# Performance work log

Measured on AMD Instinct MI355X. Metric: run time of the kernel, lower is better.

Reference implementation:

```python
import jax, jax.numpy as jnp
import numpy as np

B, S, D, H, DK, F, L, V = 4, 128, 512, 8, 64, 2048, 2, 32000
N = B * S  # nodes per side (enc and dec each)


def _pe():
    pos = np.arange(S, dtype=np.float32)[:, None]
    div = np.exp(-np.log(10000.0) * np.arange(0, D, 2, dtype=np.float32) / D)
    pe = np.zeros((S, D), dtype=np.float32)
    pe[:, 0::2] = np.sin(pos * div)
    pe[:, 1::2] = np.cos(pos * div)
    return jnp.asarray(np.tile(pe, (B, 1)))  # [N, D]


def _ln(x, g, b, eps=1e-5):
    mu = jnp.mean(x, -1, keepdims=True)
    var = jnp.mean(jnp.square(x - mu), -1, keepdims=True)
    return g * (x - mu) * jax.lax.rsqrt(var + eps) + b


def _edge_attn(q, k, v, src, dst, n_dst):
    # src_dot_dst('k','q','score') then scaled_exp, then src_mul_edge + sum scatter
    s = jnp.sum(k[src] * q[dst], -1, keepdims=True) / np.float32(np.sqrt(DK))  # [E,H,1]
    s = jnp.exp(jnp.clip(s, -10.0, 10.0))
    wv = jax.ops.segment_sum(v[src] * s, dst, num_segments=n_dst)  # [n_dst,H,DK]
    z = jax.ops.segment_sum(s, dst, num_segments=n_dst)            # [n_dst,H,1]
    return wv / z


def _attn_block(x_q, x_kv, Wq, Wk, Wv, Wo, src, dst):
    q = (x_q @ Wq).reshape(-1, H, DK)
    k = (x_kv @ Wk).reshape(-1, H, DK)
    v = (x_kv @ Wv).reshape(-1, H, DK)
    o = _edge_attn(q, k, v, src, dst, x_q.shape[0]).reshape(-1, D)
    return o @ Wo


def _forward(p, src_tok, tgt_tok, ee_src, ee_dst, dd_src, dd_dst, ed_src, ed_dst):
    (src_emb, tgt_emb, enc_Wqkv, enc_Wo, enc_ln1, enc_W1, enc_b1, enc_W2, enc_b2,
     enc_ln2, enc_lnf, dec_Wqkv, dec_Wo, dec_ln1, dec_cWq, dec_cWkv, dec_cWo,
     dec_ln2, dec_W1, dec_b1, dec_W2, dec_b2, dec_ln3, dec_lnf, gen_W, gen_b) = p
    pe = _pe()
    scale = np.float32(np.sqrt(D))
    x_e = src_emb[src_tok].reshape(N, D) * scale + pe  # token + positional embed
    x_d = tgt_emb[tgt_tok].reshape(N, D) * scale + pe
    for l in range(L):  # encoder layers (ee edges)
        xn = _ln(x_e, enc_ln1[l, 0], enc_ln1[l, 1])
        x_e = x_e + _attn_block(xn, xn, enc_Wqkv[l, 0], enc_Wqkv[l, 1], enc_Wqkv[l, 2], enc_Wo[l], ee_src, ee_dst)
        xn = _ln(x_e, enc_ln2[l, 0], enc_ln2[l, 1])
        x_e = x_e + jax.nn.relu(xn @ enc_W1[l] + enc_b1[l]) @ enc_W2[l] + enc_b2[l]
    x_e = _ln(x_e, enc_lnf[0], enc_lnf[1])
    for l in range(L):  # decoder layers: self (dd) then cross (ed)
        xn = _ln(x_d, dec_ln1[l, 0], dec_ln1[l, 1])
        x_d = x_d + _attn_block(xn, xn, dec_Wqkv[l, 0], dec_Wqkv[l, 1], dec_Wqkv[l, 2], dec_Wo[l], dd_src, dd_dst)
        xn = _ln(x_d, dec_ln2[l, 0], dec_ln2[l, 1])
        x_d = x_d + _attn_block(xn, x_e, dec_cWq[l], dec_cWkv[l, 0], dec_cWkv[l, 1], dec_cWo[l], ed_src, ed_dst)
        xn = _ln(x_d, dec_ln3[l, 0], dec_ln3[l, 1])
        x_d = x_d + jax.nn.relu(xn @ dec_W1[l] + dec_b1[l]) @ dec_W2[l] + dec_b2[l]
    x_d = _ln(x_d, dec_lnf[0], dec_lnf[1])
    return jax.nn.log_softmax(x_d @ gen_W + gen_b, axis=-1)  # generator


def setup_inputs():
    key = jax.random.key(0)
    ks = iter(jax.random.split(key, 32))
    w = lambda *shape: jax.random.normal(next(ks), shape, jnp.float32) * 0.02
    lnp = lambda n: jnp.tile(jnp.stack([jnp.ones(D), jnp.zeros(D)])[None], (n, 1, 1))
    # structured edge lists: per-sentence blocks
    i, j = np.meshgrid(np.arange(S), np.arange(S), indexing='ij')  # src pos, dst pos
    base = (np.arange(B)[:, None] * S).astype(np.int32)
    full_s = (base + i.ravel()[None, :]).ravel().astype(np.int32)
    full_d = (base + j.ravel()[None, :]).ravel().astype(np.int32)
    m = i.ravel() <= j.ravel()  # causal mask for dec self-attention
    dd_s = (base + i.ravel()[m][None, :]).ravel().astype(np.int32)
    dd_d = (base + j.ravel()[m][None, :]).ravel().astype(np.int32)
    k1, k2 = jax.random.split(next(ks))
    return dict(
        src_emb=w(V, D), tgt_emb=w(V, D),
        enc_Wqkv=w(L, 3, D, D), enc_Wo=w(L, D, D), enc_ln1=lnp(L),
        enc_W1=w(L, D, F), enc_b1=jnp.zeros((L, F)), enc_W2=w(L, F, D),
        enc_b2=jnp.zeros((L, D)), enc_ln2=lnp(L), enc_lnf=lnp(1)[0],
        dec_Wqkv=w(L, 3, D, D), dec_Wo=w(L, D, D), dec_ln1=lnp(L),
        dec_cWq=w(L, D, D), dec_cWkv=w(L, 2, D, D), dec_cWo=w(L, D, D), dec_ln2=lnp(L),
        dec_W1=w(L, D, F), dec_b1=jnp.zeros((L, F)), dec_W2=w(L, F, D),
        dec_b2=jnp.zeros((L, D)), dec_ln3=lnp(L), dec_lnf=lnp(1)[0],
        gen_W=w(D, V), gen_b=jnp.zeros((V,)),
        src_tok=jax.random.randint(k1, (B, S), 0, V, jnp.int32),
        tgt_tok=jax.random.randint(k2, (B, S), 0, V, jnp.int32),
        ee_src=jnp.asarray(full_s), ee_dst=jnp.asarray(full_d),
        dd_src=jnp.asarray(dd_s), dd_dst=jnp.asarray(dd_d),
        ed_src=jnp.asarray(full_s), ed_dst=jnp.asarray(full_d),
    )


def reference(src_emb, tgt_emb, enc_Wqkv, enc_Wo, enc_ln1, enc_W1, enc_b1, enc_W2,
              enc_b2, enc_ln2, enc_lnf, dec_Wqkv, dec_Wo, dec_ln1, dec_cWq,
              dec_cWkv, dec_cWo, dec_ln2, dec_W1, dec_b1, dec_W2, dec_b2,
              dec_ln3, dec_lnf, gen_W, gen_b, src_tok, tgt_tok, ee_src, ee_dst,
              dd_src, dd_dst, ed_src, ed_dst):
    p = (src_emb, tgt_emb, enc_Wqkv, enc_Wo, enc_ln1, enc_W1, enc_b1, enc_W2,
         enc_b2, enc_ln2, enc_lnf, dec_Wqkv, dec_Wo, dec_ln1, dec_cWq, dec_cWkv,
         dec_cWo, dec_ln2, dec_W1, dec_b1, dec_W2, dec_b2, dec_ln3, dec_lnf,
         gen_W, gen_b)
    return _forward(p, src_tok, tgt_tok, ee_src, ee_dst, dd_src, dd_dst, ed_src, ed_dst)
```

## Files before the change

### kernel.cpp

```cpp
#include <hip/hip_runtime.h>
#include <cstddef>

constexpr int cB = 4, cS = 128, cD = 512, cH = 8, cDK = 64, cF = 2048, cL = 2, cV = 32000;
constexpr int cN = cB * cS;

typedef __attribute__((ext_vector_type(8)))  short short8;
typedef __attribute__((ext_vector_type(4)))  float f32x4;
typedef __attribute__((ext_vector_type(16))) float f32x16;

__device__ __forceinline__ short f2bf(float x) {
    unsigned u = __builtin_bit_cast(unsigned, x);
    unsigned r = (u + 0x7fffu + ((u >> 16) & 1u)) >> 16;
    return (short)r;
}
__device__ __forceinline__ short f2h(float x) {
    return __builtin_bit_cast(short, (_Float16)x);
}
__device__ __forceinline__ float h2f(short s) {
    return (float)__builtin_bit_cast(_Float16, s);
}

__device__ __forceinline__ void bar_lgkm() {
    asm volatile("s_waitcnt lgkmcnt(0)" ::: "memory");
    __builtin_amdgcn_s_barrier();
    asm volatile("" ::: "memory");
}

__global__ __launch_bounds__(256) void embed_k(const float* __restrict__ e0,
                                               const int* __restrict__ t0,
                                               float* __restrict__ X0,
                                               const float* __restrict__ e1,
                                               const int* __restrict__ t1,
                                               float* __restrict__ X1)
{
    const float* emb = blockIdx.z ? e1 : e0;
    const int* tok   = blockIdx.z ? t1 : t0;
    float* X         = blockIdx.z ? X1 : X0;
    int n = blockIdx.x;
    int tid = threadIdx.x;
    int t = tok[n];
    int pos = n & (cS - 1);
    const float scale = 22.62741699796952f;
    for (int d = tid; d < cD; d += 256) {
        int i2 = d & ~1;
        float div = expf(-9.210340371976184f * (float)i2 / (float)cD);
        float arg = (float)pos * div;
        float p = (d & 1) ? cosf(arg) : sinf(arg);
        X[(long)n * cD + d] = emb[(long)t * cD + d] * scale + p;
    }
}

__global__ __launch_bounds__(256) void ln_k(const float* __restrict__ X,
                                            const float* __restrict__ g,
                                            const float* __restrict__ bta,
                                            short* __restrict__ Yb)
{
    __shared__ float red[256];
    int row = blockIdx.x, tid = threadIdx.x;
    const float* x = X + (long)row * cD;
    float v0 = x[tid], v1 = x[tid + 256];

    red[tid] = v0 + v1;
    __syncthreads();
    for (int st = 128; st > 0; st >>= 1) { if (tid < st) red[tid] += red[tid + st]; __syncthreads(); }
    float mu = red[0] * (1.0f / (float)cD);
    __syncthreads();

    float d0 = v0 - mu, d1 = v1 - mu;
    red[tid] = d0 * d0 + d1 * d1;
    __syncthreads();
    for (int st = 128; st > 0; st >>= 1) { if (tid < st) red[tid] += red[tid + st]; __syncthreads(); }
    float var = red[0] * (1.0f / (float)cD);
    float rs = rsqrtf(var + 1e-5f);

    Yb[(long)row * cD + tid]       = f2bf(g[tid]       * d0 * rs + bta[tid]);
    Yb[(long)row * cD + tid + 256] = f2bf(g[tid + 256] * d1 * rs + bta[tid + 256]);
}

struct TCP { const float* s[24]; };

__global__ __launch_bounds__(256) void tconv_k(TCP ptrs, short* __restrict__ dst,
                                               int K, int N)
{
    __shared__ float t[64][65];
    const float* s = ptrs.s[blockIdx.z];
    short* d = dst + (long)blockIdx.z * K * N;
    int k0 = blockIdx.y * 64, n0 = blockIdx.x * 64;
    int tid = threadIdx.x;
    const f32x4* s4 = (const f32x4*)s;
#pragma unroll
    for (int i = 0; i < 4; i++) {
        int lin = tid + i * 256;
        int r = lin >> 4, c4 = lin & 15;
        f32x4 v = s4[(long)(k0 + r) * (N >> 2) + (n0 >> 2) + c4];
        t[r][c4 * 4 + 0] = v[0]; t[r][c4 * 4 + 1] = v[1];
        t[r][c4 * 4 + 2] = v[2]; t[r][c4 * 4 + 3] = v[3];
    }
    __syncthreads();
#pragma unroll
    for (int i = 0; i < 2; i++) {
        int lin = tid + i * 256;
        int r = lin >> 3, c8 = lin & 7;
        short8 o;
#pragma unroll
        for (int j = 0; j < 8; j++) o[j] = f2bf(t[c8 * 8 + j][r]);
        *(short8*)&d[(long)(n0 + r) * K + k0 + c8 * 8] = o;
    }
}

template <int MR, int NR, bool LNF>
__global__ __launch_bounds__(512) void gemm8_k(
    const short* __restrict__ Abf, const float* __restrict__ Af,
    const float* __restrict__ lng, const float* __restrict__ lnb,
    const float* __restrict__ Af2, const float* __restrict__ lng2,
    const float* __restrict__ lnb2, int zsplit,
    const short* __restrict__ Bt,
    const float* __restrict__ bias, const float* __restrict__ res,
    float* __restrict__ C, short* __restrict__ Cb,
    int N, int K, int relu, long aStride, long btStride, long cStride)
{
    constexpr int BM = MR * 32, BN = NR * 32, PITCH = 136;
    constexpr int ACH = (BM * 128) / (8 * 512);
    constexpr int BCH = (BN * 128) / (8 * 512);
    static_assert(ACH >= 1 && BCH >= 1, "tile too small");
    __shared__ short As[2][BM * PITCH];
    __shared__ short Bs[2][BN * PITCH];
    __shared__ float red[4][64][MR * NR * 4];
    __shared__ float mu_s[BM], rs_s[BM];
    __shared__ float gb_s[2][LNF ? 512 : 8];

    const int z = blockIdx.z;
    const float* Afz = (LNF && z >= zsplit) ? Af2 : Af;
    const float* gz  = (LNF && z >= zsplit) ? lng2 : lng;
    const float* bz  = (LNF && z >= zsplit) ? lnb2 : lnb;
    const short* Am = Abf ? (Abf + (long)z * aStride) : nullptr;
    const short* Bm = Bt + (long)z * btStride;
    int tid = threadIdx.x;
    int lane = tid & 63, wid = tid >> 6;
    int grp = wid >> 2, quad = wid & 3;
    int wr = quad >> 1, wc = quad & 1;
    int m0 = blockIdx.y * BM, n0 = blockIdx.x * BN;
    int lrow = lane & 15, koff = (lane >> 4) * 8;
    const int Kh = K >> 1;

    if constexpr (LNF) {
        constexpr int TPR = 512 / BM;
        int r = tid / TPR, sub = tid % TPR;
        const f32x4* row4 = (const f32x4*)(Afz + (long)(m0 + r) * K);
        float s = 0.f, s2 = 0.f;
        for (int i = sub; i < (K >> 2); i += TPR) {
            f32x4 v = row4[i];
            s  += v[0] + v[1] + v[2] + v[3];
            s2 += v[0] * v[0] + v[1] * v[1] + v[2] * v[2] + v[3] * v[3];
        }
#pragma unroll
        for (int o = TPR >> 1; o > 0; o >>= 1) {
            s += __shfl_xor(s, o); s2 += __shfl_xor(s2, o);
        }
        if (sub == 0) {
            float mu = s / (float)K;
            float var = s2 / (float)K - mu * mu;
            mu_s[r] = mu; rs_s[r] = rsqrtf(var + 1e-5f);
        }
        if (tid < 512) { gb_s[0][tid] = gz[tid]; gb_s[1][tid] = bz[tid]; }
        bar_lgkm();
    }

    f32x4 acc[MR][NR];
#pragma unroll
    for (int m = 0; m < MR; m++)
#pragma unroll
        for (int n = 0; n < NR; n++) acc[m][n] = f32x4{0.f, 0.f, 0.f, 0.f};

    short8 qa0[ACH], qa1[ACH], qb0[BCH], qb1[BCH];

    auto stage = [&](int step, short8 (&qa)[ACH], short8 (&qb)[BCH]) {
#pragma unroll
        for (int i = 0; i < ACH; i++) {
            int lin = tid + i * 512, r = lin >> 4, c8 = lin & 15;
            int kg = (c8 < 8) ? (step * 64 + c8 * 8) : (Kh + step * 64 + (c8 - 8) * 8);
            if constexpr (LNF) {
                const f32x4* p = (const f32x4*)(Afz + (long)(m0 + r) * K + kg);
                f32x4 f0 = p[0], f1 = p[1];
                float mu = mu_s[r], rs = rs_s[r];
                short8 o;
#pragma unroll
                for (int j = 0; j < 4; j++)
                    o[j] = f2bf((f0[j] - mu) * rs * gb_s[0][kg + j] + gb_s[1][kg + j]);
#pragma unroll
                for (int j = 0; j < 4; j++)
                    o[4 + j] = f2bf((f1[j] - mu) * rs * gb_s[0][kg + 4 + j] + gb_s[1][kg + 4 + j]);
                qa[i] = o;
            } else {
                qa[i] = *(const short8*)&Am[(long)(m0 + r) * K + kg];
            }
        }
#pragma unroll
        for (int i = 0; i < BCH; i++) {
            int lin = tid + i * 512, r = lin >> 4, c8 = lin & 15;
            int kg = (c8 < 8) ? (step * 64 + c8 * 8) : (Kh + step * 64 + (c8 - 8) * 8);
            qb[i] = *(const short8*)&Bm[(long)(n0 + r) * K + kg];
        }
    };
    auto writeT = [&](int buf, short8 (&qa)[ACH], short8 (&qb)[BCH]) {
#pragma unroll
        for (int i = 0; i < ACH; i++) {
            int lin = tid + i * 512, r = lin >> 4, c8 = lin & 15;
            *(short8*)&As[buf][r * PITCH + c8 * 8] = qa[i];
        }
#pragma unroll
        for (int i = 0; i < BCH; i++) {
            int lin = tid + i * 512, r = lin >> 4, c8 = lin & 15;
            *(short8*)&Bs[buf][r * PITCH + c8 * 8] = qb[i];
        }
    };
    auto mfmaStep = [&](int buf) {
#pragma unroll
        for (int kk2 = 0; kk2 < 2; kk2++) {
            int kk = grp * 64 + kk2 * 32;
            short8 a[MR], b[NR];
#pragma unroll
            for (int m = 0; m < MR; m++)
                a[m] = *(const short8*)&As[buf][(wr * MR * 16 + m * 16 + lrow) * PITCH + kk + koff];
#pragma unroll
            for (int n = 0; n < NR; n++)
                b[n] = *(const short8*)&Bs[buf][(wc * NR * 16 + n * 16 + lrow) * PITCH + kk + koff];
#pragma unroll
            for (int m = 0; m < MR; m++)
#pragma unroll
                for (int n = 0; n < NR; n++)
                    acc[m][n] = __builtin_amdgcn_mfma_f32_16x16x32_bf16(a[m], b[n], acc[m][n], 0, 0, 0);
        }
    };

    const int steps = K >> 7;
    stage(0, qa0, qb0);
    if (steps > 1) stage(1, qa1, qb1);

    int st = 0;
    for (;;) {
        writeT(0, qa0, qb0);
        if (st + 2 < steps) stage(st + 2, qa0, qb0);
        bar_lgkm();
        mfmaStep(0);
        st++; if (st >= steps) break;

        writeT(1, qa1, qb1);
        if (st + 2 < steps) stage(st + 2, qa1, qb1);
        bar_lgkm();
        mfmaStep(1);
        st++; if (st >= steps) break;
    }

    __syncthreads();
    if (grp == 1) {
#pragma unroll
        for (int m = 0; m < MR; m++)
#pragma unroll
            for (int n = 0; n < NR; n++)
#pragma unroll
                for (int j = 0; j < 4; j++)
                    red[quad][lane][(m * NR + n) * 4 + j] = acc[m][n][j];
    }
    __syncthreads();
    if (grp == 0) {
#pragma unroll
        for (int m = 0; m < MR; m++) {
            int rbase = m0 + wr * MR * 16 + m * 16 + (lane >> 4) * 4;
#pragma unroll
            for (int n = 0; n < NR; n++) {
                int col = n0 + wc * NR * 16 + n * 16 + (lane & 15);
                float bv = bias ? bias[col] : 0.f;
#pragma unroll
                for (int j = 0; j < 4; j++) {
                    long row = rbase + j;
                    long off = row * N + col + (long)z * cStride;
                    float v = acc[m][n][j] + red[quad][lane][(m * NR + n) * 4 + j] + bv;
                    if (res)  v += res[off];
                    if (relu) v = fmaxf(v, 0.f);
                    if (C)  C[off] = v;
                    if (Cb) Cb[off] = f2bf(v);
                }
            }
        }
    }
}

__global__ __launch_bounds__(256) void attn_k(const short* __restrict__ Qb,
                                              const short* __restrict__ Kb,
                                              const short* __restrict__ Vb,
                                              short* __restrict__ Ob,
                                              int causMask, long sQKV, long sO)
{
    __shared__ short q_s[64 * 72];
    __shared__ short k_s[128 * 72];
    __shared__ short vt_s[64 * 128];
    __shared__ short p_s[64 * 136];
    __shared__ float z_s[64];

    int tid = threadIdx.x, lane = tid & 63, wid = tid >> 6;
    int lr = lane & 15, lg = lane >> 4;
    int h = blockIdx.x, b = blockIdx.y;
    int stream = blockIdx.z >> 1, dstBase = (blockIdx.z & 1) * 64;
    int causal = (causMask >> stream) & 1;
    const short* Q = Qb + (long)stream * sQKV;
    const short* Km = Kb + (long)stream * sQKV;
    const short* Vm = Vb + (long)stream * sQKV;
    short* O = Ob + (long)stream * sO;
    const int RS = cH * cDK;
    long qbase = ((long)b * cS + dstBase) * RS + h * cDK;
    long kbase = ((long)b * cS) * RS + h * cDK;

#pragma unroll
    for (int i = 0; i < 2; i++) {
        int lin = tid + i * 256, t = lin >> 3, c8 = lin & 7;
        *(short8*)&q_s[t * 72 + c8 * 8] = *(const short8*)&Q[qbase + (long)t * RS + c8 * 8];
    }
#pragma unroll
    for (int i = 0; i < 4; i++) {
        int lin = tid + i * 256, t = lin >> 3, c8 = lin & 7;
        *(short8*)&k_s[t * 72 + c8 * 8] = *(const short8*)&Km[kbase + (long)t * RS + c8 * 8];
    }
#pragma unroll
    for (int i = 0; i < 4; i++) {
        int lin = tid + i * 256, src = lin >> 3, c8 = lin & 7;
        short8 v = *(const short8*)&Vm[kbase + (long)src * RS + c8 * 8];
#pragma unroll
        for (int j = 0; j < 8; j++) {
            int dk = c8 * 8 + j;
            int g = (src >> 3) ^ (dk >> 3);
            vt_s[dk * 128 + g * 8 + (src & 7)] = v[j];
        }
    }
    bar_lgkm();

    f32x4 sacc[8];
#pragma unroll
    for (int n = 0; n < 8; n++) sacc[n] = f32x4{0.f, 0.f, 0.f, 0.f};
#pragma unroll
    for (int kk = 0; kk < 64; kk += 32) {
        short8 a = *(const short8*)&q_s[(wid * 16 + lr) * 72 + kk + lg * 8];
#pragma unroll
        for (int n = 0; n < 8; n++) {
            short8 bf = *(const short8*)&k_s[(n * 16 + lr) * 72 + kk + lg * 8];
            sacc[n] = __builtin_amdgcn_mfma_f32_16x16x32_bf16(a, bf, sacc[n], 0, 0, 0);
        }
    }
    float z[4] = {0.f, 0.f, 0.f, 0.f};
#pragma unroll
    for (int n = 0; n < 8; n++) {
        int src = n * 16 + lr;
#pragma unroll
        for (int j = 0; j < 4; j++) {
            int dst = dstBase + wid * 16 + lg * 4 + j;
            float s = sacc[n][j] * 0.125f;
            s = __expf(fminf(fmaxf(s, -10.f), 10.f));
            if (causal && src > dst) s = 0.f;
            sacc[n][j] = s;
            z[j] += s;
        }
    }
#pragma unroll
    for (int j = 0; j < 4; j++) {
        z[j] += __shfl_xor(z[j], 1); z[j] += __shfl_xor(z[j], 2);
        z[j] += __shfl_xor(z[j], 4); z[j] += __shfl_xor(z[j], 8);
    }
#pragma unroll
    for (int n = 0; n < 8; n++) {
        int src = n * 16 + lr;
#pragma unroll
        for (int j = 0; j < 4; j++)
            p_s[(wid * 16 + lg * 4 + j) * 136 + src] = f2bf(sacc[n][j]);
    }
    if (lr == 0) {
#pragma unroll
        for (int j = 0; j < 4; j++) z_s[wid * 16 + lg * 4 + j] = z[j];
    }
    bar_lgkm();

    f32x4 oacc[4];
#pragma unroll
    for (int n = 0; n < 4; n++) oacc[n] = f32x4{0.f, 0.f, 0.f, 0.f};
#pragma unroll
    for (int kk = 0; kk < 128; kk += 32) {
        int dkr = wid * 16 + lr;
        int g = ((kk >> 3) + lg) ^ (dkr >> 3);
        short8 a = *(const short8*)&vt_s[dkr * 128 + g * 8];
#pragma unroll
        for (int n = 0; n < 4; n++) {
            short8 bf = *(const short8*)&p_s[(n * 16 + lr) * 136 + kk + lg * 8];
            oacc[n] = __builtin_amdgcn_mfma_f32_16x16x32_bf16(a, bf, oacc[n], 0, 0, 0);
        }
    }
#pragma unroll
    for (int n = 0; n < 4; n++) {
        int dl = n * 16 + lr;
        float zz = z_s[dl];
#pragma unroll
        for (int j = 0; j < 4; j++) {
            int dk = wid * 16 + lg * 4 + j;
            O[qbase + (long)dl * RS + dk] = f2bf(oacc[n][j] / zz);
        }
    }
}

__global__ __launch_bounds__(256) void gen32_k(
    const short* __restrict__ A, const float* __restrict__ Bw,
    const float* __restrict__ bias, short* __restrict__ Ch, int N, int K)
{
    constexpr int PA = 72, PB = 132;
    __shared__ short As[128 * PA];
    __shared__ float Bsf[64 * PB];

    int bx = blockIdx.x, by = blockIdx.y;
    {
        int nb = gridDim.x * gridDim.y;
        int bid = by * gridDim.x + bx;
        int w = (bid & 7) * (nb >> 3) + (bid >> 3);
        by = w % gridDim.y; bx = w / gridDim.y;
    }
    int tid = threadIdx.x;
    int lane = tid & 63, wid = tid >> 6;
    int wr = wid >> 1, wc = wid & 1;
    int m0 = by * 128, n0 = bx * 128;
    int l31 = lane & 31, l5 = lane >> 5;

    f32x16 acc[2][2];
#pragma unroll
    for (int m = 0; m < 2; m++)
#pragma unroll
        for (int n = 0; n < 2; n++)
#pragma unroll
            for (int r = 0; r < 16; r++) acc[m][n][r] = 0.f;

    short8 qa0[4], qa1[4];
    f32x4  qb0[8], qb1[8];
    auto stage = [&](int k0, short8 (&qa)[4], f32x4 (&qb)[8]) {
#pragma unroll
        for (int i = 0; i < 4; i++) {
            int lin = tid + i * 256, r = lin >> 3, c8 = lin & 7;
            qa[i] = *(const short8*)&A[(long)(m0 + r) * K + k0 + c8 * 8];
        }
#pragma unroll
        for (int i = 0; i < 8; i++) {
            int lin = tid + i * 256, kr = lin >> 5, c4 = lin & 31;
            qb[i] = *(const f32x4*)&Bw[(long)(k0 + kr) * N + n0 + c4 * 4];
        }
    };
    auto writeT = [&](short8 (&qa)[4], f32x4 (&qb)[8]) {
#pragma unroll
        for (int i = 0; i < 4; i++) {
            int lin = tid + i * 256, r = lin >> 3, c8 = lin & 7;
            *(short8*)&As[r * PA + c8 * 8] = qa[i];
        }
#pragma unroll
        for (int i = 0; i < 8; i++) {
            int lin = tid + i * 256, kr = lin >> 5, c4 = lin & 31;
            *(f32x4*)&Bsf[kr * PB + c4 * 4] = qb[i];
        }
    };
    auto mfmaStep = [&]() {
#pragma unroll
        for (int kk = 0; kk < 64; kk += 16) {
            short8 a[2], b[2];
#pragma unroll
            for (int m = 0; m < 2; m++)
                a[m] = *(const short8*)&As[(wr * 64 + m * 32 + l31) * PA + kk + l5 * 8];
#pragma unroll
            for (int n = 0; n < 2; n++) {
                int col = wc * 64 + n * 32 + l31;
#pragma unroll
                for (int j = 0; j < 8; j++)
                    b[n][j] = f2bf(Bsf[(kk + l5 * 8 + j) * PB + col]);
            }
#pragma unroll
            for (int m = 0; m < 2; m++)
#pragma unroll
                for (int n = 0; n < 2; n++)
                    acc[m][n] = __builtin_amdgcn_mfma_f32_32x32x16_bf16(a[m], b[n], acc[m][n], 0, 0, 0);
        }
    };

    const int steps = K >> 6;
    stage(0, qa0, qb0);
    stage(64, qa1, qb1);
    int st = 0;
    for (;;) {
        if (st) bar_lgkm();
        writeT(qa0, qb0);
        if (st + 2 < steps) stage((st + 2) * 64, qa0, qb0);
        bar_lgkm();
        mfmaStep();
        st++; if (st >= steps) break;

        bar_lgkm();
        writeT(qa1, qb1);
        if (st + 2 < steps) stage((st + 2) * 64, qa1, qb1);
        bar_lgkm();
        mfmaStep();
        st++; if (st >= steps) break;
    }

#pragma unroll
    for (int m = 0; m < 2; m++) {
#pragma unroll
        for (int n = 0; n < 2; n++) {
            int col = n0 + wc * 64 + n * 32 + l31;
            float bv = bias[col];
#pragma unroll
            for (int r = 0; r < 16; r++) {
                int row = m0 + wr * 64 + m * 32 + (r & 3) + 8 * (r >> 2) + 4 * l5;
                Ch[(long)row * N + col] = f2h(acc[m][n][r] + bv);
            }
        }
    }
}

__global__ __launch_bounds__(256) void lsm_k(const short* __restrict__ L16,
                                             float* __restrict__ Out)
{
    __shared__ float rm[256], rs[256];
    int row = blockIdx.x, tid = threadIdx.x;
    const short8* x8 = (const short8*)(L16 + (long)row * cV);
    float* o = Out + (long)row * cV;
    constexpr int NV = cV / 8;

    float m = -1e30f, s = 0.f;
    for (int i = tid; i < NV; i += 256) {
        short8 v = x8[i];
        float f[8];
#pragma unroll
        for (int j = 0; j < 8; j++) f[j] = h2f(v[j]);
        float cm = f[0];
#pragma unroll
        for (int j = 1; j < 8; j++) cm = fmaxf(cm, f[j]);
        float nm = fmaxf(m, cm);
        float a = 0.f;
#pragma unroll
        for (int j = 0; j < 8; j++) a += __expf(f[j] - nm);
        s = s * __expf(m - nm) + a;
        m = nm;
    }
    rm[tid] = m; rs[tid] = s;
    __syncthreads();
    for (int st = 128; st > 0; st >>= 1) {
        if (tid < st) {
            float m2 = rm[tid + st], s2 = rs[tid + st];
            float nm = fmaxf(rm[tid], m2);
            rs[tid] = rs[tid] * __expf(rm[tid] - nm) + s2 * __expf(m2 - nm);
            rm[tid] = nm;
        }
        __syncthreads();
    }
    float lse = rm[0] + __logf(rs[0]);

    for (int i = tid; i < NV; i += 256) {
        short8 v = x8[i];
        f32x4 o0, o1;
#pragma unroll
        for (int j = 0; j < 4; j++) o0[j] = h2f(v[j]) - lse;
#pragma unroll
        for (int j = 0; j < 4; j++) o1[j] = h2f(v[4 + j]) - lse;
        *(f32x4*)&o[i * 8]     = o0;
        *(f32x4*)&o[i * 8 + 4] = o1;
    }
}

extern "C" void kernel_launch(void* const* d_in, const int* in_sizes, int n_in,
                              void* d_out, int out_size, void* d_ws, size_t ws_size,
                              hipStream_t stream)
{
    const float* src_emb  = (const float*)d_in[0];
    const float* tgt_emb  = (const float*)d_in[1];
    const float* enc_Wqkv = (const float*)d_in[2];
    const float* enc_Wo   = (const float*)d_in[3];
    const float* enc_ln1  = (const float*)d_in[4];
    const float* enc_W1   = (const float*)d_in[5];
    const float* enc_b1   = (const float*)d_in[6];
    const float* enc_W2   = (const float*)d_in[7];
    const float* enc_b2   = (const float*)d_in[8];
    const float* enc_ln2  = (const float*)d_in[9];
    const float* enc_lnf  = (const float*)d_in[10];
    const float* dec_Wqkv = (const float*)d_in[11];
    const float* dec_Wo   = (const float*)d_in[12];
    const float* dec_ln1  = (const float*)d_in[13];
    const float* dec_cWq  = (const float*)d_in[14];
    const float* dec_cWkv = (const float*)d_in[15];
    const float* dec_cWo  = (const float*)d_in[16];
    const float* dec_ln2  = (const float*)d_in[17];
    const float* dec_W1   = (const float*)d_in[18];
    const float* dec_b1   = (const float*)d_in[19];
    const float* dec_W2   = (const float*)d_in[20];
    const float* dec_b2   = (const float*)d_in[21];
    const float* dec_ln3  = (const float*)d_in[22];
    const float* dec_lnf  = (const float*)d_in[23];
    const float* gen_W    = (const float*)d_in[24];
    const float* gen_b    = (const float*)d_in[25];
    const int* src_tok    = (const int*)d_in[26];
    const int* tgt_tok    = (const int*)d_in[27];

    const long ND = (long)cN * cD;
    const long DD = (long)cD * cD;
    const long DF = (long)cD * cF;

    float* x_e = (float*)d_ws;
    float* x_d = x_e + ND;

    short* qkv6  = (short*)(x_d + ND);
    short* ob2   = qkv6 + 6 * ND;
    short* hb_bf = ob2 + 2 * ND;
    short* kvc   = hb_bf + (long)cN * cF;
    short* xn_bf = kvc + 4 * ND;
    short* wDD  = xn_bf + ND;
    short* wDF  = wDD + 24 * DD;
    short* wFD  = wDF + 4 * DF;
    short* lg16 = wFD + 4 * DF;

    {
        TCP p{};
        int i = 0;
        for (int j = 0; j < 3; j++) p.s[i++] = enc_Wqkv + (long)j * DD;
        for (int j = 0; j < 3; j++) p.s[i++] = dec_Wqkv + (long)j * DD;
        p.s[i++] = enc_Wo; p.s[i++] = dec_Wo;
        for (int j = 3; j < 6; j++) p.s[i++] = enc_Wqkv + (long)j * DD;
        for (int j = 3; j < 6; j++) p.s[i++] = dec_Wqkv + (long)j * DD;
        p.s[i++] = enc_Wo + DD; p.s[i++] = dec_Wo + DD;
        for (int j = 0; j < 2; j++) p.s[i++] = dec_cWq  + (long)j * DD;
        for (int j = 0; j < 4; j++) p.s[i++] = dec_cWkv + (long)j * DD;
        for (int j = 0; j < 2; j++) p.s[i++] = dec_cWo  + (long)j * DD;
        tconv_k<<<dim3(cD / 64, cD / 64, 24), 256, 0, stream>>>(p, wDD, cD, cD);
    }
    {
        TCP p{};
        p.s[0] = enc_W1; p.s[1] = enc_W1 + DF; p.s[2] = dec_W1; p.s[3] = dec_W1 + DF;
        tconv_k<<<dim3(cF / 64, cD / 64, 4), 256, 0, stream>>>(p, wDF, cD, cF);
    }
    {
        TCP p{};
        p.s[0] = enc_W2; p.s[1] = enc_W2 + DF; p.s[2] = dec_W2; p.s[3] = dec_W2 + DF;
        tconv_k<<<dim3(cD / 64, cF / 64, 4), 256, 0, stream>>>(p, wFD, cF, cD);
    }

    embed_k<<<dim3(cN, 1, 2), 256, 0, stream>>>(src_emb, src_tok, x_e,
                                                tgt_emb, tgt_tok, x_d);

    dim3 gDD(cD / 32, cN / 32);
    dim3 gFFN1(cF / 64, cN / 64);

    gemm8_k<1, 1, true><<<dim3(cD / 32, cN / 32, 6), 512, 0, stream>>>(
        nullptr, x_e, enc_ln1, enc_ln1 + cD,
        x_d, dec_ln1, dec_ln1 + cD, 3,
        wDD, nullptr, nullptr, nullptr, qkv6, cD, cD, 0, 0, DD, ND);
    attn_k<<<dim3(cH, cB, 4), 256, 0, stream>>>(
        qkv6, qkv6 + ND, qkv6 + 2 * ND, ob2, 0b10, 3 * ND, ND);
    gemm8_k<1, 1, false><<<dim3(cD / 32, cN / 32, 2), 512, 0, stream>>>(
        ob2, nullptr, nullptr, nullptr, nullptr, nullptr, nullptr, 99,
        wDD + 6 * DD, nullptr, x_e, x_e, nullptr, cD, cD, 0, ND, DD, ND);

    gemm8_k<2, 2, true><<<gFFN1, 512, 0, stream>>>(
        nullptr, x_e, enc_ln2, enc_ln2 + cD, nullptr, nullptr, nullptr, 99,
        wDF, enc_b1, nullptr, nullptr, hb_bf, cF, cD, 1, 0, 0, 0);
    gemm8_k<1, 1, false><<<gDD, 512, 0, stream>>>(
        hb_bf, nullptr, nullptr, nullptr, nullptr, nullptr, nullptr, 99,
        wFD, enc_b2, x_e, x_e, nullptr, cD, cF, 0, 0, 0, 0);

    gemm8_k<1, 1, true><<<dim3(cD / 32, cN / 32, 3), 512, 0, stream>>>(
        nullptr, x_e, enc_ln1 + 2 * cD, enc_ln1 + 3 * cD,
        nullptr, nullptr, nullptr, 99,
        wDD + 8 * DD, nullptr, nullptr, nullptr, qkv6, cD, cD, 0, 0, DD, ND);
    attn_k<<<dim3(cH, cB, 2), 256, 0, stream>>>(
        qkv6, qkv6 + ND, qkv6 + 2 * ND, ob2, 0, 0, 0);
    gemm8_k<1, 1, false><<<gDD, 512, 0, stream>>>(
        ob2, nullptr, nullptr, nullptr, nullptr, nullptr, nullptr, 99,
        wDD + 14 * DD, nullptr, x_e, x_e, nullptr, cD, cD, 0, 0, 0, 0);
    gemm8_k<2, 2, true><<<gFFN1, 512, 0, stream>>>(
        nullptr, x_e, enc_ln2 + 2 * cD, enc_ln2 + 3 * cD,
        nullptr, nullptr, nullptr, 99,
        wDF + DF, enc_b1 + cF, nullptr, nullptr, hb_bf, cF, cD, 1, 0, 0, 0);
    gemm8_k<1, 1, false><<<gDD, 512, 0, stream>>>(
        hb_bf, nullptr, nullptr, nullptr, nullptr, nullptr, nullptr, 99,
        wFD + DF, enc_b2 + cD, x_e, x_e, nullptr, cD, cF, 0, 0, 0, 0);

    gemm8_k<1, 1, true><<<dim3(cD / 32, cN / 32, 4), 512, 0, stream>>>(
        nullptr, x_e, enc_lnf, enc_lnf + cD, nullptr, nullptr, nullptr, 99,
        wDD + 18 * DD, nullptr, nullptr, nullptr, kvc, cD, cD, 0, 0, DD, ND);

    for (int l = 0; l < cL; l++) {
        if (l == 1) {
            gemm8_k<1, 1, true><<<dim3(cD / 32, cN / 32, 3), 512, 0, stream>>>(
                nullptr, x_d, dec_ln1 + 2 * cD, dec_ln1 + 3 * cD,
                nullptr, nullptr, nullptr, 99,
                wDD + 11 * DD, nullptr, nullptr, nullptr, qkv6, cD, cD, 0, 0, DD, ND);
            attn_k<<<dim3(cH, cB, 2), 256, 0, stream>>>(
                qkv6, qkv6 + ND, qkv6 + 2 * ND, ob2, 1, 0, 0);
            gemm8_k<1, 1, false><<<gDD, 512, 0, stream>>>(
                ob2, nullptr, nullptr, nullptr, nullptr, nullptr, nullptr, 99,
                wDD + 15 * DD, nullptr, x_d, x_d, nullptr, cD, cD, 0, 0, 0, 0);
        }
        gemm8_k<1, 1, true><<<gDD, 512, 0, stream>>>(
            nullptr, x_d, dec_ln2 + (long)(2 * l) * cD, dec_ln2 + (long)(2 * l + 1) * cD,
            nullptr, nullptr, nullptr, 99,
            wDD + (long)(16 + l) * DD, nullptr, nullptr, nullptr, qkv6, cD, cD, 0, 0, 0, 0);
        attn_k<<<dim3(cH, cB, 2), 256, 0, stream>>>(
            qkv6, kvc + (long)(2 * l) * ND, kvc + (long)(2 * l + 1) * ND, ob2, 0, 0, 0);
        gemm8_k<1, 1, false><<<gDD, 512, 0, stream>>>(
            ob2, nullptr, nullptr, nullptr, nullptr, nullptr, nullptr, 99,
            wDD + (long)(22 + l) * DD, nullptr, x_d, x_d, nullptr, cD, cD, 0, 0, 0, 0);
        gemm8_k<2, 2, true><<<gFFN1, 512, 0, stream>>>(
            nullptr, x_d, dec_ln3 + (long)(2 * l) * cD, dec_ln3 + (long)(2 * l + 1) * cD,
            nullptr, nullptr, nullptr, 99,
            wDF + (long)(2 + l) * DF, dec_b1 + (long)l * cF, nullptr, nullptr, hb_bf,
            cF, cD, 1, 0, 0, 0);
        gemm8_k<1, 1, false><<<gDD, 512, 0, stream>>>(
            hb_bf, nullptr, nullptr, nullptr, nullptr, nullptr, nullptr, 99,
            wFD + (long)(2 + l) * DF, dec_b2 + (long)l * cD, x_d, x_d, nullptr,
            cD, cF, 0, 0, 0, 0);
    }

    ln_k<<<cN, 256, 0, stream>>>(x_d, dec_lnf, dec_lnf + cD, xn_bf);
    gen32_k<<<dim3(cV / 128, cN / 128), 256, 0, stream>>>(
        xn_bf, gen_W, gen_b, lg16, cV, cD);
    lsm_k<<<cN, 256, 0, stream>>>(lg16, (float*)d_out);
}
```

Before: 343.0 us.

## Specialize GEMM on K, prefetch all stages, pre-transpose generator weights, merge decoder q-projection

```diff
diff --git a/kernel.cpp b/kernel.cpp
--- a/kernel.cpp
+++ b/kernel.cpp
@@ -108,7 +108,7 @@
     }
 }
 
-template <int MR, int NR, bool LNF>
+template <int MR, int NR, bool LNF, int KSTEPS>
 __global__ __launch_bounds__(512) void gemm8_k(
     const short* __restrict__ Abf, const float* __restrict__ Af,
     const float* __restrict__ lng, const float* __restrict__ lnb,
@@ -117,12 +117,14 @@
     const short* __restrict__ Bt,
     const float* __restrict__ bias, const float* __restrict__ res,
     float* __restrict__ C, short* __restrict__ Cb,
-    int N, int K, int relu, long aStride, long btStride, long cStride)
+    int N, int relu, long aStride, long btStride, long cStride)
 {
+    constexpr int K = KSTEPS * 128;
     constexpr int BM = MR * 32, BN = NR * 32, PITCH = 136;
     constexpr int ACH = (BM * 128) / (8 * 512);
     constexpr int BCH = (BN * 128) / (8 * 512);
     static_assert(ACH >= 1 && BCH >= 1, "tile too small");
+    static_assert(!LNF || KSTEPS <= 4, "LNF only on short-K path");
     __shared__ short As[2][BM * PITCH];
     __shared__ short Bs[2][BN * PITCH];
     __shared__ float red[4][64][MR * NR * 4];
@@ -143,58 +145,28 @@
     int lrow = lane & 15, koff = (lane >> 4) * 8;
     const int Kh = K >> 1;
 
-    if constexpr (LNF) {
-        constexpr int TPR = 512 / BM;
-        int r = tid / TPR, sub = tid % TPR;
-        const f32x4* row4 = (const f32x4*)(Afz + (long)(m0 + r) * K);
-        float s = 0.f, s2 = 0.f;
-        for (int i = sub; i < (K >> 2); i += TPR) {
-            f32x4 v = row4[i];
-            s  += v[0] + v[1] + v[2] + v[3];
-            s2 += v[0] * v[0] + v[1] * v[1] + v[2] * v[2] + v[3] * v[3];
-        }
-#pragma unroll
-        for (int o = TPR >> 1; o > 0; o >>= 1) {
-            s += __shfl_xor(s, o); s2 += __shfl_xor(s2, o);
-        }
-        if (sub == 0) {
-            float mu = s / (float)K;
-            float var = s2 / (float)K - mu * mu;
-            mu_s[r] = mu; rs_s[r] = rsqrtf(var + 1e-5f);
-        }
-        if (tid < 512) { gb_s[0][tid] = gz[tid]; gb_s[1][tid] = bz[tid]; }
-        bar_lgkm();
-    }
-
     f32x4 acc[MR][NR];
 #pragma unroll
     for (int m = 0; m < MR; m++)
 #pragma unroll
         for (int n = 0; n < NR; n++) acc[m][n] = f32x4{0.f, 0.f, 0.f, 0.f};
 
-    short8 qa0[ACH], qa1[ACH], qb0[BCH], qb1[BCH];
-
-    auto stage = [&](int step, short8 (&qa)[ACH], short8 (&qb)[BCH]) {
+    constexpr int FAN = LNF ? ACH * 2 : 1;
+
+    auto stageA = [&](int step, short8 (&qa)[ACH], f32x4 (&fa)[FAN]) {
 #pragma unroll
         for (int i = 0; i < ACH; i++) {
             int lin = tid + i * 512, r = lin >> 4, c8 = lin & 15;
             int kg = (c8 < 8) ? (step * 64 + c8 * 8) : (Kh + step * 64 + (c8 - 8) * 8);
             if constexpr (LNF) {
                 const f32x4* p = (const f32x4*)(Afz + (long)(m0 + r) * K + kg);
-                f32x4 f0 = p[0], f1 = p[1];
-                float mu = mu_s[r], rs = rs_s[r];
-                short8 o;
-#pragma unroll
-                for (int j = 0; j < 4; j++)
-                    o[j] = f2bf((f0[j] - mu) * rs * gb_s[0][kg + j] + gb_s[1][kg + j]);
-#pragma unroll
-                for (int j = 0; j < 4; j++)
-                    o[4 + j] = f2bf((f1[j] - mu) * rs * gb_s[0][kg + 4 + j] + gb_s[1][kg + 4 + j]);
-                qa[i] = o;
+                fa[2 * i] = p[0]; fa[2 * i + 1] = p[1];
             } else {
                 qa[i] = *(const short8*)&Am[(long)(m0 + r) * K + kg];
             }
         }
+    };
+    auto stageB = [&](int step, short8 (&qb)[BCH]) {
 #pragma unroll
         for (int i = 0; i < BCH; i++) {
             int lin = tid + i * 512, r = lin >> 4, c8 = lin & 15;
@@ -202,11 +174,25 @@
             qb[i] = *(const short8*)&Bm[(long)(n0 + r) * K + kg];
         }
     };
-    auto writeT = [&](int buf, short8 (&qa)[ACH], short8 (&qb)[BCH]) {
+    auto writeT = [&](int buf, int step, short8 (&qa)[ACH], f32x4 (&fa)[FAN],
+                      short8 (&qb)[BCH]) {
 #pragma unroll
         for (int i = 0; i < ACH; i++) {
             int lin = tid + i * 512, r = lin >> 4, c8 = lin & 15;
-            *(short8*)&As[buf][r * PITCH + c8 * 8] = qa[i];
+            if constexpr (LNF) {
+                int kg = (c8 < 8) ? (step * 64 + c8 * 8) : (Kh + step * 64 + (c8 - 8) * 8);
+                float mu = mu_s[r], rs = rs_s[r];
+                short8 o;
+#pragma unroll
+                for (int j = 0; j < 4; j++)
+                    o[j] = f2bf((fa[2 * i][j] - mu) * rs * gb_s[0][kg + j] + gb_s[1][kg + j]);
+#pragma unroll
+                for (int j = 0; j < 4; j++)
+                    o[4 + j] = f2bf((fa[2 * i + 1][j] - mu) * rs * gb_s[0][kg + 4 + j] + gb_s[1][kg + 4 + j]);
+                *(short8*)&As[buf][r * PITCH + c8 * 8] = o;
+            } else {
+                *(short8*)&As[buf][r * PITCH + c8 * 8] = qa[i];
+            }
         }
 #pragma unroll
         for (int i = 0; i < BCH; i++) {
@@ -232,24 +218,66 @@
                     acc[m][n] = __builtin_amdgcn_mfma_f32_16x16x32_bf16(a[m], b[n], acc[m][n], 0, 0, 0);
         }
     };
-
-    const int steps = K >> 7;
-    stage(0, qa0, qb0);
-    if (steps > 1) stage(1, qa1, qb1);
-
-    int st = 0;
-    for (;;) {
-        writeT(0, qa0, qb0);
-        if (st + 2 < steps) stage(st + 2, qa0, qb0);
-        bar_lgkm();
-        mfmaStep(0);
-        st++; if (st >= steps) break;
-
-        writeT(1, qa1, qb1);
-        if (st + 2 < steps) stage(st + 2, qa1, qb1);
-        bar_lgkm();
-        mfmaStep(1);
-        st++; if (st >= steps) break;
+    auto lnProlog = [&]() {
+        if constexpr (LNF) {
+            constexpr int TPR = 512 / BM;
+            int r = tid / TPR, sub = tid % TPR;
+            const f32x4* row4 = (const f32x4*)(Afz + (long)(m0 + r) * K);
+            float s = 0.f, s2 = 0.f;
+            for (int i = sub; i < (K >> 2); i += TPR) {
+                f32x4 v = row4[i];
+                s  += v[0] + v[1] + v[2] + v[3];
+                s2 += v[0] * v[0] + v[1] * v[1] + v[2] * v[2] + v[3] * v[3];
+            }
+#pragma unroll
+            for (int o = TPR >> 1; o > 0; o >>= 1) {
+                s += __shfl_xor(s, o); s2 += __shfl_xor(s2, o);
+            }
+            if (sub == 0) {
+                float mu = s / (float)K;
+                float var = s2 / (float)K - mu * mu;
+                mu_s[r] = mu; rs_s[r] = rsqrtf(var + 1e-5f);
+            }
+            if (tid < 512) { gb_s[0][tid] = gz[tid]; gb_s[1][tid] = bz[tid]; }
+            bar_lgkm();
+        }
+    };
+
+    if constexpr (KSTEPS <= 4) {
+        short8 qa[KSTEPS][ACH], qb[KSTEPS][BCH];
+        f32x4 fa[LNF ? KSTEPS : 1][FAN];
+#pragma unroll
+        for (int s = 0; s < KSTEPS; s++) {
+            stageA(s, qa[s], fa[LNF ? s : 0]);
+            stageB(s, qb[s]);
+        }
+        lnProlog();
+#pragma unroll
+        for (int s = 0; s < KSTEPS; s++) {
+            writeT(s & 1, s, qa[s], fa[LNF ? s : 0], qb[s]);
+            bar_lgkm();
+            mfmaStep(s & 1);
+            if (s + 1 < KSTEPS) bar_lgkm();
+        }
+    } else {
+        short8 qa0[ACH], qa1[ACH], qb0[BCH], qb1[BCH];
+        f32x4 fdum[FAN];
+        stageA(0, qa0, fdum); stageB(0, qb0);
+        stageA(1, qa1, fdum); stageB(1, qb1);
+        int st = 0;
+        for (;;) {
+            writeT(0, st, qa0, fdum, qb0);
+            if (st + 2 < KSTEPS) { stageA(st + 2, qa0, fdum); stageB(st + 2, qb0); }
+            bar_lgkm();
+            mfmaStep(0);
+            st++; if (st >= KSTEPS) break;
+
+            writeT(1, st, qa1, fdum, qb1);
+            if (st + 2 < KSTEPS) { stageA(st + 2, qa1, fdum); stageB(st + 2, qb1); }
+            bar_lgkm();
+            mfmaStep(1);
+            st++; if (st >= KSTEPS) break;
+        }
     }
 
     __syncthreads();
@@ -405,12 +433,13 @@
 }
 
 __global__ __launch_bounds__(256) void gen32_k(
-    const short* __restrict__ A, const float* __restrict__ Bw,
+    const short* __restrict__ A, const short* __restrict__ Bt,
     const float* __restrict__ bias, short* __restrict__ Ch, int N, int K)
 {
-    constexpr int PA = 72, PB = 132;
-    __shared__ short As[128 * PA];
-    __shared__ float Bsf[64 * PB];
+    constexpr int PITCH = 72;
+    constexpr int ACH = 4, BCH = 4;
+    __shared__ short As[2][128 * PITCH];
+    __shared__ short Bs[2][128 * PITCH];
 
     int bx = blockIdx.x, by = blockIdx.y;
     {
@@ -433,46 +462,41 @@
 #pragma unroll
             for (int r = 0; r < 16; r++) acc[m][n][r] = 0.f;
 
-    short8 qa0[4], qa1[4];
-    f32x4  qb0[8], qb1[8];
-    auto stage = [&](int k0, short8 (&qa)[4], f32x4 (&qb)[8]) {
-#pragma unroll
-        for (int i = 0; i < 4; i++) {
+    short8 qa0[ACH], qa1[ACH], qb0[BCH], qb1[BCH];
+    auto stage = [&](int k0, short8 (&qa)[ACH], short8 (&qb)[BCH]) {
+#pragma unroll
+        for (int i = 0; i < ACH; i++) {
             int lin = tid + i * 256, r = lin >> 3, c8 = lin & 7;
             qa[i] = *(const short8*)&A[(long)(m0 + r) * K + k0 + c8 * 8];
         }
 #pragma unroll
-        for (int i = 0; i < 8; i++) {
-            int lin = tid + i * 256, kr = lin >> 5, c4 = lin & 31;
-            qb[i] = *(const f32x4*)&Bw[(long)(k0 + kr) * N + n0 + c4 * 4];
+        for (int i = 0; i < BCH; i++) {
+            int lin = tid + i * 256, r = lin >> 3, c8 = lin & 7;
+            qb[i] = *(const short8*)&Bt[(long)(n0 + r) * K + k0 + c8 * 8];
         }
     };
-    auto writeT = [&](short8 (&qa)[4], f32x4 (&qb)[8]) {
-#pragma unroll
-        for (int i = 0; i < 4; i++) {
+    auto writeT = [&](int buf, short8 (&qa)[ACH], short8 (&qb)[BCH]) {
+#pragma unroll
+        for (int i = 0; i < ACH; i++) {
             int lin = tid + i * 256, r = lin >> 3, c8 = lin & 7;
-            *(short8*)&As[r * PA + c8 * 8] = qa[i];
-        }
-#pragma unroll
-        for (int i = 0; i < 8; i++) {
-            int lin = tid + i * 256, kr = lin >> 5, c4 = lin & 31;
-            *(f32x4*)&Bsf[kr * PB + c4 * 4] = qb[i];
+            *(short8*)&As[buf][r * PITCH + c8 * 8] = qa[i];
+        }
+#pragma unroll
+        for (int i = 0; i < BCH; i++) {
+            int lin = tid + i * 256, r = lin >> 3, c8 = lin & 7;
+            *(short8*)&Bs[buf][r * PITCH + c8 * 8] = qb[i];
         }
     };
-    auto mfmaStep = [&]() {
+    auto mfmaStep = [&](int buf) {
 #pragma unroll
         for (int kk = 0; kk < 64; kk += 16) {
             short8 a[2], b[2];
 #pragma unroll
             for (int m = 0; m < 2; m++)
-                a[m] = *(const short8*)&As[(wr * 64 + m * 32 + l31) * PA + kk + l5 * 8];
-#pragma unroll
-            for (int n = 0; n < 2; n++) {
-                int col = wc * 64 + n * 32 + l31;
-#pragma unroll
-                for (int j = 0; j < 8; j++)
-                    b[n][j] = f2bf(Bsf[(kk + l5 * 8 + j) * PB + col]);
-            }
+                a[m] = *(const short8*)&As[buf][(wr * 64 + m * 32 + l31) * PITCH + kk + l5 * 8];
+#pragma unroll
+            for (int n = 0; n < 2; n++)
+                b[n] = *(const short8*)&Bs[buf][(wc * 64 + n * 32 + l31) * PITCH + kk + l5 * 8];
 #pragma unroll
             for (int m = 0; m < 2; m++)
 #pragma unroll
@@ -486,18 +510,16 @@
     stage(64, qa1, qb1);
     int st = 0;
     for (;;) {
-        if (st) bar_lgkm();
-        writeT(qa0, qb0);
+        writeT(0, qa0, qb0);
         if (st + 2 < steps) stage((st + 2) * 64, qa0, qb0);
         bar_lgkm();
-        mfmaStep();
+        mfmaStep(0);
         st++; if (st >= steps) break;
 
-        bar_lgkm();
-        writeT(qa1, qb1);
+        writeT(1, qa1, qb1);
         if (st + 2 < steps) stage((st + 2) * 64, qa1, qb1);
         bar_lgkm();
-        mfmaStep();
+        mfmaStep(1);
         st++; if (st >= steps) break;
     }
 
@@ -614,7 +636,8 @@
     short* wDD  = xn_bf + ND;
     short* wDF  = wDD + 24 * DD;
     short* wFD  = wDF + 4 * DF;
-    short* lg16 = wFD + 4 * DF;
+    short* genT = wFD + 4 * DF;
+    short* lg16 = genT + (long)cD * cV;
 
     {
         TCP p{};
@@ -623,9 +646,11 @@
         for (int j = 0; j < 3; j++) p.s[i++] = dec_Wqkv + (long)j * DD;
         p.s[i++] = enc_Wo; p.s[i++] = dec_Wo;
         for (int j = 3; j < 6; j++) p.s[i++] = enc_Wqkv + (long)j * DD;
+        p.s[i++] = dec_cWq;
         for (int j = 3; j < 6; j++) p.s[i++] = dec_Wqkv + (long)j * DD;
-        p.s[i++] = enc_Wo + DD; p.s[i++] = dec_Wo + DD;
-        for (int j = 0; j < 2; j++) p.s[i++] = dec_cWq  + (long)j * DD;
+        p.s[i++] = enc_Wo + DD;
+        p.s[i++] = dec_Wo + DD;
+        p.s[i++] = dec_cWq + DD;
         for (int j = 0; j < 4; j++) p.s[i++] = dec_cWkv + (long)j * DD;
         for (int j = 0; j < 2; j++) p.s[i++] = dec_cWo  + (long)j * DD;
         tconv_k<<<dim3(cD / 64, cD / 64, 24), 256, 0, stream>>>(p, wDD, cD, cD);
@@ -640,6 +665,11 @@
         p.s[0] = enc_W2; p.s[1] = enc_W2 + DF; p.s[2] = dec_W2; p.s[3] = dec_W2 + DF;
         tconv_k<<<dim3(cD / 64, cF / 64, 4), 256, 0, stream>>>(p, wFD, cF, cD);
     }
+    {
+        TCP p{};
+        p.s[0] = gen_W;
+        tconv_k<<<dim3(cV / 64, cD / 64, 1), 256, 0, stream>>>(p, genT, cD, cV);
+    }
 
     embed_k<<<dim3(cN, 1, 2), 256, 0, stream>>>(src_emb, src_tok, x_e,
                                                 tgt_emb, tgt_tok, x_d);
@@ -647,78 +677,84 @@
     dim3 gDD(cD / 32, cN / 32);
     dim3 gFFN1(cF / 64, cN / 64);
 
-    gemm8_k<1, 1, true><<<dim3(cD / 32, cN / 32, 6), 512, 0, stream>>>(
+    gemm8_k<1, 1, true, 4><<<dim3(cD / 32, cN / 32, 6), 512, 0, stream>>>(
         nullptr, x_e, enc_ln1, enc_ln1 + cD,
         x_d, dec_ln1, dec_ln1 + cD, 3,
-        wDD, nullptr, nullptr, nullptr, qkv6, cD, cD, 0, 0, DD, ND);
+        wDD, nullptr, nullptr, nullptr, qkv6, cD, 0, 0, DD, ND);
     attn_k<<<dim3(cH, cB, 4), 256, 0, stream>>>(
         qkv6, qkv6 + ND, qkv6 + 2 * ND, ob2, 0b10, 3 * ND, ND);
-    gemm8_k<1, 1, false><<<dim3(cD / 32, cN / 32, 2), 512, 0, stream>>>(
+    gemm8_k<1, 1, false, 4><<<dim3(cD / 32, cN / 32, 2), 512, 0, stream>>>(
         ob2, nullptr, nullptr, nullptr, nullptr, nullptr, nullptr, 99,
-        wDD + 6 * DD, nullptr, x_e, x_e, nullptr, cD, cD, 0, ND, DD, ND);
-
-    gemm8_k<2, 2, true><<<gFFN1, 512, 0, stream>>>(
+        wDD + 6 * DD, nullptr, x_e, x_e, nullptr, cD, 0, ND, DD, ND);
+
+    gemm8_k<2, 2, true, 4><<<gFFN1, 512, 0, stream>>>(
         nullptr, x_e, enc_ln2, enc_ln2 + cD, nullptr, nullptr, nullptr, 99,
-        wDF, enc_b1, nullptr, nullptr, hb_bf, cF, cD, 1, 0, 0, 0);
-    gemm8_k<1, 1, false><<<gDD, 512, 0, stream>>>(
+        wDF, enc_b1, nullptr, nullptr, hb_bf, cF, 1, 0, 0, 0);
+    gemm8_k<1, 1, false, 16><<<gDD, 512, 0, stream>>>(
         hb_bf, nullptr, nullptr, nullptr, nullptr, nullptr, nullptr, 99,
-        wFD, enc_b2, x_e, x_e, nullptr, cD, cF, 0, 0, 0, 0);
-
-    gemm8_k<1, 1, true><<<dim3(cD / 32, cN / 32, 3), 512, 0, stream>>>(
+        wFD, enc_b2, x_e, x_e, nullptr, cD, 0, 0, 0, 0);
+
+    gemm8_k<1, 1, true, 4><<<dim3(cD / 32, cN / 32, 4), 512, 0, stream>>>(
         nullptr, x_e, enc_ln1 + 2 * cD, enc_ln1 + 3 * cD,
-        nullptr, nullptr, nullptr, 99,
-        wDD + 8 * DD, nullptr, nullptr, nullptr, qkv6, cD, cD, 0, 0, DD, ND);
+        x_d, dec_ln2, dec_ln2 + cD, 3,
+        wDD + 8 * DD, nullptr, nullptr, nullptr, qkv6, cD, 0, 0, DD, ND);
     attn_k<<<dim3(cH, cB, 2), 256, 0, stream>>>(
         qkv6, qkv6 + ND, qkv6 + 2 * ND, ob2, 0, 0, 0);
-    gemm8_k<1, 1, false><<<gDD, 512, 0, stream>>>(
+    gemm8_k<1, 1, false, 4><<<gDD, 512, 0, stream>>>(
         ob2, nullptr, nullptr, nullptr, nullptr, nullptr, nullptr, 99,
-        wDD + 14 * DD, nullptr, x_e, x_e, nullptr, cD, cD, 0, 0, 0, 0);
-    gemm8_k<2, 2, true><<<gFFN1, 512, 0, stream>>>(
+        wDD + 15 * DD, nullptr, x_e, x_e, nullptr, cD, 0, 0, 0, 0);
+    gemm8_k<2, 2, true, 4><<<gFFN1, 512, 0, stream>>>(
         nullptr, x_e, enc_ln2 + 2 * cD, enc_ln2 + 3 * cD,
         nullptr, nullptr, nullptr, 99,
-        wDF + DF, enc_b1 + cF, nullptr, nullptr, hb_bf, cF, cD, 1, 0, 0, 0);
-    gemm8_k<1, 1, false><<<gDD, 512, 0, stream>>>(
+        wDF + DF, enc_b1 + cF, nullptr, nullptr, hb_bf, cF, 1, 0, 0, 0);
+    gemm8_k<1, 1, false, 16><<<gDD, 512, 0, stream>>>(
         hb_bf, nullptr, nullptr, nullptr, nullptr, nullptr, nullptr, 99,
-        wFD + DF, enc_b2 + cD, x_e, x_e, nullptr, cD, cF, 0, 0, 0, 0);
-
-    gemm8_k<1, 1, true><<<dim3(cD / 32, cN / 32, 4), 512, 0, stream>>>(
+        wFD + DF, enc_b2 + cD, x_e, x_e, nullptr, cD, 0, 0, 0, 0);
+
+    gemm8_k<1, 1, true, 4><<<dim3(cD / 32, cN / 32, 4), 512, 0, stream>>>(
         nullptr, x_e, enc_lnf, enc_lnf + cD, nullptr, nullptr, nullptr, 99,
-        wDD + 18 * DD, nullptr, nullptr, nullptr, kvc, cD, cD, 0, 0, DD, ND);
-
-    for (int l = 0; l < cL; l++) {
-        if (l == 1) {
-            gemm8_k<1, 1, true><<<dim3(cD / 32, cN / 32, 3), 512, 0, stream>>>(
-                nullptr, x_d, dec_ln1 + 2 * cD, dec_ln1 + 3 * cD,
-                nullptr, nullptr, nullptr, 99,
-                wDD + 11 * DD, nullptr, nullptr, nullptr, qkv6, cD, cD, 0, 0, DD, ND);
-            attn_k<<<dim3(cH, cB, 2), 256, 0, stream>>>(
-                qkv6, qkv6 + ND, qkv6 + 2 * ND, ob2, 1, 0, 0);
-            gemm8_k<1, 1, false><<<gDD, 512, 0, stream>>>(
-                ob2, nullptr, nullptr, nullptr, nullptr, nullptr, nullptr, 99,
-                wDD + 15 * DD, nullptr, x_d, x_d, nullptr, cD, cD, 0, 0, 0, 0);
-        }
-        gemm8_k<1, 1, true><<<gDD, 512, 0, stream>>>(
-            nullptr, x_d, dec_ln2 + (long)(2 * l) * cD, dec_ln2 + (long)(2 * l + 1) * cD,
-            nullptr, nullptr, nullptr, 99,
-            wDD + (long)(16 + l) * DD, nullptr, nullptr, nullptr, qkv6, cD, cD, 0, 0, 0, 0);
-        attn_k<<<dim3(cH, cB, 2), 256, 0, stream>>>(
-            qkv6, kvc + (long)(2 * l) * ND, kvc + (long)(2 * l + 1) * ND, ob2, 0, 0, 0);
-        gemm8_k<1, 1, false><<<gDD, 512, 0, stream>>>(
-            ob2, nullptr, nullptr, nullptr, nullptr, nullptr, nullptr, 99,
-            wDD + (long)(22 + l) * DD, nullptr, x_d, x_d, nullptr, cD, cD, 0, 0, 0, 0);
-        gemm8_k<2, 2, true><<<gFFN1, 512, 0, stream>>>(
-            nullptr, x_d, dec_ln3 + (long)(2 * l) * cD, dec_ln3 + (long)(2 * l + 1) * cD,
-            nullptr, nullptr, nullptr, 99,
-            wDF + (long)(2 + l) * DF, dec_b1 + (long)l * cF, nullptr, nullptr, hb_bf,
-            cF, cD, 1, 0, 0, 0);
-        gemm8_k<1, 1, false><<<gDD, 512, 0, stream>>>(
-            hb_bf, nullptr, nullptr, nullptr, nullptr, nullptr, nullptr, 99,
-            wFD + (long)(2 + l) * DF, dec_b2 + (long)l * cD, x_d, x_d, nullptr,
-            cD, cF, 0, 0, 0, 0);
-    }
+        wDD + 18 * DD, nullptr, nullptr, nullptr, kvc, cD, 0, 0, DD, ND);
+
+    attn_k<<<dim3(cH, cB, 2), 256, 0, stream>>>(
+        qkv6 + 3 * ND, kvc, kvc + ND, ob2, 0, 0, 0);
+    gemm8_k<1, 1, false, 4><<<gDD, 512, 0, stream>>>(
+        ob2, nullptr, nullptr, nullptr, nullptr, nullptr, nullptr, 99,
+        wDD + 22 * DD, nullptr, x_d, x_d, nullptr, cD, 0, 0, 0, 0);
+    gemm8_k<2, 2, true, 4><<<gFFN1, 512, 0, stream>>>(
+        nullptr, x_d, dec_ln3, dec_ln3 + cD, nullptr, nullptr, nullptr, 99,
+        wDF + 2 * DF, dec_b1, nullptr, nullptr, hb_bf, cF, 1, 0, 0, 0);
+    gemm8_k<1, 1, false, 16><<<gDD, 512, 0, stream>>>(
+        hb_bf, nullptr, nullptr, nullptr, nullptr, nullptr, nullptr, 99,
+        wFD + 2 * DF, dec_b2, x_d, x_d, nullptr, cD, 0, 0, 0, 0);
+
+    gemm8_k<1, 1, true, 4><<<dim3(cD / 32, cN / 32, 3), 512, 0, stream>>>(
+        nullptr, x_d, dec_ln1 + 2 * cD, dec_ln1 + 3 * cD,
+        nullptr, nullptr, nullptr, 99,
+        wDD + 12 * DD, nullptr, nullptr, nullptr, qkv6, cD, 0, 0, DD, ND);
+    attn_k<<<dim3(cH, cB, 2), 256, 0, stream>>>(
+        qkv6, qkv6 + ND, qkv6 + 2 * ND, ob2, 1, 0, 0);
+    gemm8_k<1, 1, false, 4><<<gDD, 512, 0, stream>>>(
+        ob2, nullptr, nullptr, nullptr, nullptr, nullptr, nullptr, 99,
+        wDD + 16 * DD, nullptr, x_d, x_d, nullptr, cD, 0, 0, 0, 0);
+    gemm8_k<1, 1, true, 4><<<gDD, 512, 0, stream>>>(
+        nullptr, x_d, dec_ln2 + 2 * cD, dec_ln2 + 3 * cD,
+        nullptr, nullptr, nullptr, 99,
+        wDD + 17 * DD, nullptr, nullptr, nullptr, qkv6, cD, 0, 0, 0, 0);
+    attn_k<<<dim3(cH, cB, 2), 256, 0, stream>>>(
+        qkv6, kvc + 2 * ND, kvc + 3 * ND, ob2, 0, 0, 0);
+    gemm8_k<1, 1, false, 4><<<gDD, 512, 0, stream>>>(
+        ob2, nullptr, nullptr, nullptr, nullptr, nullptr, nullptr, 99,
+        wDD + 23 * DD, nullptr, x_d, x_d, nullptr, cD, 0, 0, 0, 0);
+    gemm8_k<2, 2, true, 4><<<gFFN1, 512, 0, stream>>>(
+        nullptr, x_d, dec_ln3 + 2 * cD, dec_ln3 + 3 * cD,
+        nullptr, nullptr, nullptr, 99,
+        wDF + 3 * DF, dec_b1 + cF, nullptr, nullptr, hb_bf, cF, 1, 0, 0, 0);
+    gemm8_k<1, 1, false, 16><<<gDD, 512, 0, stream>>>(
+        hb_bf, nullptr, nullptr, nullptr, nullptr, nullptr, nullptr, 99,
+        wFD + 3 * DF, dec_b2 + cD, x_d, x_d, nullptr, cD, 0, 0, 0, 0);
 
     ln_k<<<cN, 256, 0, stream>>>(x_d, dec_lnf, dec_lnf + cD, xn_bf);
     gen32_k<<<dim3(cV / 128, cN / 128), 256, 0, stream>>>(
-        xn_bf, gen_W, gen_b, lg16, cV, cD);
+        xn_bf, genT, gen_b, lg16, cV, cD);
     lsm_k<<<cN, 256, 0, stream>>>(lg16, (float*)d_out);
 }
```

New measurement: 308.7 us. 1.11x faster.
